# Performance work log

Hardware: AMD Instinct MI355X
Metric: run time of the kernel (lower is better)

The kernel has to match this reference:

```python
import jax, jax.numpy as jnp
import numpy as np

D_MODEL = 1024
NUM_HEADS = 16
HEAD_DIM = D_MODEL // NUM_HEADS


def setup_inputs() -> dict:
    key = jax.random.key(0)
    ks = jax.random.split(key, 5)
    x = jax.random.normal(ks[0], (2, 2048, D_MODEL), dtype=jnp.float32)
    # torch.nn.Linear default init ~ U(-1/sqrt(fan_in), 1/sqrt(fan_in)); scale roughly
    s = 1.0 / np.sqrt(D_MODEL)
    W_qkv = jax.random.uniform(ks[1], (D_MODEL, 3 * D_MODEL), jnp.float32, -s, s)
    b_qkv = jax.random.uniform(ks[2], (3 * D_MODEL,), jnp.float32, -s, s)
    W_out = jax.random.uniform(ks[3], (D_MODEL, D_MODEL), jnp.float32, -s, s)
    b_out = jax.random.uniform(ks[4], (D_MODEL,), jnp.float32, -s, s)
    return {"x": x, "W_qkv": W_qkv, "b_qkv": b_qkv, "W_out": W_out, "b_out": b_out}


def reference(x, W_qkv, b_qkv, W_out, b_out):
    B, S, D = x.shape
    H, Hd = NUM_HEADS, HEAD_DIM
    qkv = x @ W_qkv + b_qkv                      # [B,S,3D]
    q, k, v = jnp.split(qkv, 3, axis=-1)
    def split_heads(t):
        return t.reshape(B, S, H, Hd).transpose(0, 2, 1, 3)  # [B,H,S,Hd]
    q, k, v = split_heads(q), split_heads(k), split_heads(v)
    scores = jnp.einsum('bhqd,bhkd->bhqk', q, k) / jnp.sqrt(jnp.float32(Hd))
    weights = jax.nn.softmax(scores, axis=-1)
    attn = jnp.einsum('bhqk,bhkd->bhqd', weights, v)
    attn = attn.transpose(0, 2, 1, 3).reshape(B, S, D)
    return attn @ W_out + b_out
```

## Files before the change

### kernel.cpp

```cpp
#include <hip/hip_runtime.h>
#include <hip/hip_bf16.h>

#define DMODEL 1024
#define NH 16
#define HD 64
#define SEQ 2048
#define BATCH 2
#define BH (BATCH * NH)
#define MTOT (BATCH * SEQ)

typedef _Float16 f16x8 __attribute__((ext_vector_type(8)));
typedef _Float16 f16x4 __attribute__((ext_vector_type(4)));
typedef _Float16 f16x2 __attribute__((ext_vector_type(2)));
typedef float f32x4 __attribute__((ext_vector_type(4)));
typedef float f32x16 __attribute__((ext_vector_type(16)));

__device__ __forceinline__ void gload_lds16(const void* g, void* l) {
  __builtin_amdgcn_global_load_lds((const __attribute__((address_space(1))) unsigned*)g,
                                   (__attribute__((address_space(3))) unsigned*)l, 16, 0, 0);
}

__global__ __launch_bounds__(256) void cvt_f2h(const float* __restrict__ in,
                                               _Float16* __restrict__ out, int n8) {
  const int i = blockIdx.x * 256 + threadIdx.x;
  if (i < n8) {
    const float4 a = ((const float4*)in)[i * 2];
    const float4 b = ((const float4*)in)[i * 2 + 1];
    f16x8 o = {(_Float16)a.x, (_Float16)a.y, (_Float16)a.z, (_Float16)a.w,
               (_Float16)b.x, (_Float16)b.y, (_Float16)b.z, (_Float16)b.w};
    *(f16x8*)&out[(size_t)i * 8] = o;
  }
}

__global__ __launch_bounds__(256) void cvt_transpose(const float* __restrict__ W,
                                                     _Float16* __restrict__ Wt,
                                                     int N, int K) {
  __shared__ float Ls[64][65];
  const int k0 = blockIdx.y * 64, n0 = blockIdx.x * 64;
  const int t = threadIdx.x;
  const int r = t >> 2, c4 = (t & 3) * 16;
#pragma unroll
  for (int j = 0; j < 4; ++j) {
    const float4 v = *(const float4*)&W[(size_t)(k0 + r) * N + n0 + c4 + j * 4];
    Ls[r][c4 + j * 4 + 0] = v.x;
    Ls[r][c4 + j * 4 + 1] = v.y;
    Ls[r][c4 + j * 4 + 2] = v.z;
    Ls[r][c4 + j * 4 + 3] = v.w;
  }
  __syncthreads();
  f16x8 o0, o1;
#pragma unroll
  for (int j = 0; j < 8; ++j) {
    o0[j] = (_Float16)Ls[c4 + j][r];
    o1[j] = (_Float16)Ls[c4 + 8 + j][r];
  }
  *(f16x8*)&Wt[(size_t)(n0 + r) * K + k0 + c4] = o0;
  *(f16x8*)&Wt[(size_t)(n0 + r) * K + k0 + c4 + 8] = o1;
}

__global__ __launch_bounds__(256) void qkv_mm(const _Float16* __restrict__ A,
                                              const _Float16* __restrict__ Bt,
                                              const float* __restrict__ bias,
                                              _Float16* __restrict__ qh,
                                              _Float16* __restrict__ kh,
                                              _Float16* __restrict__ vh) {
  __shared__ __align__(16) _Float16 As[128 * 64];
  __shared__ __align__(16) _Float16 Bs[128 * 64];
  const int t = threadIdx.x;
  const int w = t >> 6, lane = t & 63;
  const int g = lane >> 4, lr = lane & 15;
  const int m0 = blockIdx.y * 128, n0 = blockIdx.x * 128;
  const int wr = w >> 1, wc = w & 1;
  const int srow = (lane >> 3);
  const int col8 = (lane & 7) * 8;
  f32x4 acc[4][4] = {};

  for (int k0 = 0; k0 < DMODEL; k0 += 64) {
    __syncthreads();
#pragma unroll
    for (int i = 0; i < 4; ++i) {
      const int row = w * 32 + i * 8 + srow;
      gload_lds16(A + (size_t)(m0 + row) * DMODEL + k0 + col8, &As[(w * 4 + i) * 512]);
      gload_lds16(Bt + (size_t)(n0 + row) * DMODEL + k0 + col8, &Bs[(w * 4 + i) * 512]);
    }
    __syncthreads();
#pragma unroll
    for (int ks = 0; ks < 2; ++ks) {
      f16x8 af[4], bf[4];
#pragma unroll
      for (int mi = 0; mi < 4; ++mi)
        af[mi] = *(const f16x8*)&As[(wr * 64 + mi * 16 + lr) * 64 + ks * 32 + g * 8];
#pragma unroll
      for (int ni = 0; ni < 4; ++ni)
        bf[ni] = *(const f16x8*)&Bs[(wc * 64 + ni * 16 + lr) * 64 + ks * 32 + g * 8];
#pragma unroll
      for (int mi = 0; mi < 4; ++mi)
#pragma unroll
        for (int ni = 0; ni < 4; ++ni)
          acc[mi][ni] = __builtin_amdgcn_mfma_f32_16x16x32_f16(af[mi], bf[ni], acc[mi][ni], 0, 0, 0);
    }
  }

#pragma unroll
  for (int ni = 0; ni < 4; ++ni) {
    const int n = n0 + wc * 64 + ni * 16 + lr;
    const float bn = bias[n];
    const int which = n >> 10, d = n & 1023, h = d >> 6, hd = d & 63;
    _Float16* dst = which == 0 ? qh : which == 1 ? kh : vh;
    const float scale = which == 0 ? 0.125f : 1.0f;
#pragma unroll
    for (int mi = 0; mi < 4; ++mi)
#pragma unroll
      for (int r = 0; r < 4; ++r) {
        const int m = m0 + wr * 64 + mi * 16 + g * 4 + r;
        const int bb = m >> 11, ss = m & 2047;
        dst[((size_t)(bb * NH + h) * SEQ + ss) * HD + hd] =
            (_Float16)((acc[mi][ni][r] + bn) * scale);
      }
  }
}

__global__ __launch_bounds__(256, 2) void attn_fused(const _Float16* __restrict__ qh,
                                                     const _Float16* __restrict__ kh,
                                                     const _Float16* __restrict__ vh,
                                                     _Float16* __restrict__ ao) {
  __shared__ __align__(16) _Float16 Vt[64][76];
  const int t = threadIdx.x;
  const int lane = t & 63, w = t >> 6;
  const int q = lane & 31, hi = lane >> 5;
  const int bh = blockIdx.y;
  const int q0 = blockIdx.x * 128 + w * 32;
  const _Float16* Qp = qh + (size_t)bh * SEQ * HD;
  const _Float16* Kp = kh + (size_t)bh * SEQ * HD;
  const _Float16* Vp = vh + (size_t)bh * SEQ * HD;

  f16x8 qf[4];
#pragma unroll
  for (int ks = 0; ks < 4; ++ks)
    qf[ks] = *(const f16x8*)(Qp + (size_t)(q0 + q) * HD + ks * 16 + hi * 8);

  f32x16 o0 = {}, o1 = {};
  float mrun = -3e30f, lrun = 0.f;

  const int skv = t & 63;
  const int sq4 = t >> 6;

  for (int kv0 = 0; kv0 < SEQ; kv0 += 64) {
    const f16x8 sv0 = *(const f16x8*)(Vp + (size_t)(kv0 + skv) * HD + sq4 * 16);
    const f16x8 sv1 = *(const f16x8*)(Vp + (size_t)(kv0 + skv) * HD + sq4 * 16 + 8);
    __syncthreads();
#pragma unroll
    for (int e = 0; e < 8; ++e) {
      Vt[sq4 * 16 + e][skv] = sv0[e];
      Vt[sq4 * 16 + 8 + e][skv] = sv1[e];
    }

    f32x16 s0 = {}, s1 = {};
#pragma unroll
    for (int ks = 0; ks < 4; ++ks) {
      const f16x8 k0 = *(const f16x8*)(Kp + (size_t)(kv0 + q) * HD + ks * 16 + hi * 8);
      const f16x8 k1 = *(const f16x8*)(Kp + (size_t)(kv0 + 32 + q) * HD + ks * 16 + hi * 8);
      s0 = __builtin_amdgcn_mfma_f32_32x32x16_f16(k0, qf[ks], s0, 0, 0, 0);
      s1 = __builtin_amdgcn_mfma_f32_32x32x16_f16(k1, qf[ks], s1, 0, 0, 0);
    }

    float tm[16];
#pragma unroll
    for (int r = 0; r < 16; ++r) tm[r] = fmaxf(s0[r], s1[r]);
#pragma unroll
    for (int d = 8; d > 0; d >>= 1)
#pragma unroll
      for (int r = 0; r < d; ++r) tm[r] = fmaxf(tm[r], tm[r + d]);
    float mx = fmaxf(tm[0], __shfl_xor(tm[0], 32));
    const float mnew = fmaxf(mrun, mx);
    const float corr = __expf(mrun - mnew);
    mrun = mnew;
#pragma unroll
    for (int r = 0; r < 16; ++r) {
      s0[r] = __expf(s0[r] - mnew);
      s1[r] = __expf(s1[r] - mnew);
    }
    float ts[16];
#pragma unroll
    for (int r = 0; r < 16; ++r) ts[r] = s0[r] + s1[r];
#pragma unroll
    for (int d = 8; d > 0; d >>= 1)
#pragma unroll
      for (int r = 0; r < d; ++r) ts[r] += ts[r + d];
    float rs = ts[0] + __shfl_xor(ts[0], 32);
    lrun = lrun * corr + rs;
#pragma unroll
    for (int r = 0; r < 16; ++r) {
      o0[r] *= corr;
      o1[r] *= corr;
    }

    __syncthreads();

#pragma unroll
    for (int ks = 0; ks < 4; ++ks) {
      const int base = 8 * (ks & 1);
      unsigned u0, u1, u2, u3;
#pragma unroll
      for (int w01 = 0; w01 < 2; ++w01) {
        float a0, a1, b0, b1;
        if (ks < 2) {
          a0 = s0[base + 2 * w01];     a1 = s0[base + 2 * w01 + 1];
          b0 = s0[base + 4 + 2 * w01]; b1 = s0[base + 4 + 2 * w01 + 1];
        } else {
          a0 = s1[base + 2 * w01];     a1 = s1[base + 2 * w01 + 1];
          b0 = s1[base + 4 + 2 * w01]; b1 = s1[base + 4 + 2 * w01 + 1];
        }
        f16x2 hm0; hm0[0] = (_Float16)a0; hm0[1] = (_Float16)a1;
        f16x2 hm1; hm1[0] = (_Float16)b0; hm1[1] = (_Float16)b1;
        unsigned Pm0, Pm1;
        __builtin_memcpy(&Pm0, &hm0, 4);
        __builtin_memcpy(&Pm1, &hm1, 4);
        const unsigned local = hi ? Pm1 : Pm0;
        const unsigned sent = hi ? Pm0 : Pm1;
        const unsigned cross = __shfl_xor(sent, 32);
        const unsigned wa = hi ? cross : local;
        const unsigned wb = hi ? local : cross;
        if (w01 == 0) { u0 = wa; u2 = wb; } else { u1 = wa; u3 = wb; }
      }
      unsigned ww[4] = {u0, u1, u2, u3};
      f16x8 pb;
      __builtin_memcpy(&pb, ww, 16);
      const f16x8 va0 = *(const f16x8*)&Vt[0 + q][ks * 16 + hi * 8];
      const f16x8 va1 = *(const f16x8*)&Vt[32 + q][ks * 16 + hi * 8];
      o0 = __builtin_amdgcn_mfma_f32_32x32x16_f16(va0, pb, o0, 0, 0, 0);
      o1 = __builtin_amdgcn_mfma_f32_32x32x16_f16(va1, pb, o1, 0, 0, 0);
    }
  }

  const float invl = 1.0f / lrun;
  _Float16* aob = ao + (size_t)bh * SEQ * HD + (size_t)(q0 + q) * HD;
#pragma unroll
  for (int m = 0; m < 4; ++m) {
    f16x4 v0, v1;
#pragma unroll
    for (int s2 = 0; s2 < 4; ++s2) {
      v0[s2] = (_Float16)(o0[4 * m + s2] * invl);
      v1[s2] = (_Float16)(o1[4 * m + s2] * invl);
    }
    *(f16x4*)(aob + 8 * m + 4 * hi) = v0;
    *(f16x4*)(aob + 32 + 8 * m + 4 * hi) = v1;
  }
}

__global__ __launch_bounds__(256) void out_mm(const _Float16* __restrict__ Ah,
                                              const _Float16* __restrict__ Bt,
                                              const float* __restrict__ bias,
                                              float* __restrict__ out) {
  __shared__ __align__(16) _Float16 As[128 * 64];
  __shared__ __align__(16) _Float16 Bs[128 * 64];
  const int t = threadIdx.x;
  const int w = t >> 6, lane = t & 63;
  const int g = lane >> 4, lr = lane & 15;
  const int m0 = blockIdx.y * 128, n0 = blockIdx.x * 128;
  const int wr = w >> 1, wc = w & 1;
  const int srow = (lane >> 3);
  const int col8 = (lane & 7) * 8;
  f32x4 acc[4][4] = {};

  for (int k0 = 0; k0 < DMODEL; k0 += 64) {
    const int h = k0 >> 6;
    __syncthreads();
#pragma unroll
    for (int i = 0; i < 4; ++i) {
      const int row = w * 32 + i * 8 + srow;
      const int m = m0 + row;
      const int bb = m >> 11, ss = m & 2047;
      gload_lds16(Ah + ((size_t)(bb * NH + h) * SEQ + ss) * HD + col8, &As[(w * 4 + i) * 512]);
      gload_lds16(Bt + (size_t)(n0 + row) * DMODEL + k0 + col8, &Bs[(w * 4 + i) * 512]);
    }
    __syncthreads();
#pragma unroll
    for (int ks = 0; ks < 2; ++ks) {
      f16x8 af[4], bf[4];
#pragma unroll
      for (int mi = 0; mi < 4; ++mi)
        af[mi] = *(const f16x8*)&As[(wr * 64 + mi * 16 + lr) * 64 + ks * 32 + g * 8];
#pragma unroll
      for (int ni = 0; ni < 4; ++ni)
        bf[ni] = *(const f16x8*)&Bs[(wc * 64 + ni * 16 + lr) * 64 + ks * 32 + g * 8];
#pragma unroll
      for (int mi = 0; mi < 4; ++mi)
#pragma unroll
        for (int ni = 0; ni < 4; ++ni)
          acc[mi][ni] = __builtin_amdgcn_mfma_f32_16x16x32_f16(af[mi], bf[ni], acc[mi][ni], 0, 0, 0);
    }
  }

#pragma unroll
  for (int ni = 0; ni < 4; ++ni) {
    const int n = n0 + wc * 64 + ni * 16 + lr;
    const float bn = bias[n];
#pragma unroll
    for (int mi = 0; mi < 4; ++mi)
#pragma unroll
      for (int r = 0; r < 4; ++r) {
        const int m = m0 + wr * 64 + mi * 16 + g * 4 + r;
        out[(size_t)m * DMODEL + n] = acc[mi][ni][r] + bn;
      }
  }
}

extern "C" void kernel_launch(void* const* d_in, const int* in_sizes, int n_in,
                              void* d_out, int out_size, void* d_ws, size_t ws_size,
                              hipStream_t stream) {
  const float* x = (const float*)d_in[0];
  const float* Wqkv = (const float*)d_in[1];
  const float* bqkv = (const float*)d_in[2];
  const float* Wout = (const float*)d_in[3];
  const float* bout = (const float*)d_in[4];
  float* out = (float*)d_out;

  char* ws = (char*)d_ws;
  const size_t MB = 1u << 20;
  _Float16* Xh = (_Float16*)(ws);
  _Float16* qh = (_Float16*)(ws + 8 * MB);
  _Float16* kh = (_Float16*)(ws + 16 * MB);
  _Float16* vh = (_Float16*)(ws + 24 * MB);
  _Float16* Wtq = (_Float16*)(ws + 32 * MB);
  _Float16* Wto = (_Float16*)(ws + 38 * MB + 512 * 1024);
  _Float16* attnh = Xh;

  cvt_f2h<<<dim3(MTOT * DMODEL / 8 / 256), 256, 0, stream>>>(x, Xh, MTOT * DMODEL / 8);
  cvt_transpose<<<dim3(3072 / 64, DMODEL / 64), 256, 0, stream>>>(Wqkv, Wtq, 3072, DMODEL);
  cvt_transpose<<<dim3(DMODEL / 64, DMODEL / 64), 256, 0, stream>>>(Wout, Wto, DMODEL, DMODEL);
  qkv_mm<<<dim3(3072 / 128, MTOT / 128), 256, 0, stream>>>(Xh, Wtq, bqkv, qh, kh, vh);
  attn_fused<<<dim3(SEQ / 128, BH), 256, 0, stream>>>(qh, kh, vh, attnh);
  out_mm<<<dim3(DMODEL / 128, MTOT / 128), 256, 0, stream>>>(attnh, Wto, bout, out);
}
```

Before: 253.9 us.

## Software-pipeline attention loop with double-buffered V and K prefetch in registers

Restructures the attention kernel's KV loop into a two-stage ping-pong. The next tile's K and V are prefetched into registers while the current tile's QK^T and softmax run, and V is double-buffered in LDS, leaving one barrier per tile instead of two. The Q scale now folds in log2(e) so exp2f replaces __expf, and the running max is only rescaled when a block's max exceeds it by more than a threshold (lazy rescaling). s_setprio is also raised around the MFMA groups. In exchange the kernel holds many more prefetch registers, which may reduce occupancy, and the lazy rescale lets unnormalized exponentials grow up to 2^8.

```diff
diff --git a/kernel.cpp b/kernel.cpp
--- a/kernel.cpp
+++ b/kernel.cpp
@@ -107,7 +107,7 @@
     const float bn = bias[n];
     const int which = n >> 10, d = n & 1023, h = d >> 6, hd = d & 63;
     _Float16* dst = which == 0 ? qh : which == 1 ? kh : vh;
-    const float scale = which == 0 ? 0.125f : 1.0f;
+    const float scale = which == 0 ? 0.18033688011f : 1.0f;
 #pragma unroll
     for (int mi = 0; mi < 4; ++mi)
 #pragma unroll
@@ -120,11 +120,125 @@
   }
 }
 
+__device__ __forceinline__ void load_k(const _Float16* Kp, int kv0, int q, int hi,
+                                       f16x8 (&kr)[8]) {
+#pragma unroll
+  for (int ks = 0; ks < 4; ++ks) {
+    kr[2 * ks] = *(const f16x8*)(Kp + (size_t)(kv0 + q) * HD + ks * 16 + hi * 8);
+    kr[2 * ks + 1] = *(const f16x8*)(Kp + (size_t)(kv0 + 32 + q) * HD + ks * 16 + hi * 8);
+  }
+}
+
+__device__ __forceinline__ void load_v(const _Float16* Vp, int kv0, int skv, int sq4,
+                                       f16x8 (&vr)[2]) {
+  vr[0] = *(const f16x8*)(Vp + (size_t)(kv0 + skv) * HD + sq4 * 16);
+  vr[1] = *(const f16x8*)(Vp + (size_t)(kv0 + skv) * HD + sq4 * 16 + 8);
+}
+
+__device__ __forceinline__ void store_v(_Float16 (*Vt)[76], int skv, int sq4,
+                                        const f16x8 (&vr)[2]) {
+#pragma unroll
+  for (int e = 0; e < 8; ++e) {
+    Vt[sq4 * 16 + e][skv] = vr[0][e];
+    Vt[sq4 * 16 + 8 + e][skv] = vr[1][e];
+  }
+}
+
+__device__ __forceinline__ void qkt(const f16x8 (&kr)[8], const f16x8 (&qf)[4],
+                                    f32x16& s0, f32x16& s1) {
+  s0 = {};
+  s1 = {};
+  __builtin_amdgcn_s_setprio(1);
+#pragma unroll
+  for (int ks = 0; ks < 4; ++ks) {
+    s0 = __builtin_amdgcn_mfma_f32_32x32x16_f16(kr[2 * ks], qf[ks], s0, 0, 0, 0);
+    s1 = __builtin_amdgcn_mfma_f32_32x32x16_f16(kr[2 * ks + 1], qf[ks], s1, 0, 0, 0);
+  }
+  __builtin_amdgcn_s_setprio(0);
+}
+
+__device__ __forceinline__ void softmax_update(f32x16& s0, f32x16& s1, float& mrun,
+                                               float& lrun, f32x16& o0, f32x16& o1) {
+  float tm[16];
+#pragma unroll
+  for (int r = 0; r < 16; ++r) tm[r] = fmaxf(s0[r], s1[r]);
+#pragma unroll
+  for (int d = 8; d > 0; d >>= 1)
+#pragma unroll
+    for (int r = 0; r < d; ++r) tm[r] = fmaxf(tm[r], tm[r + d]);
+  const float mx = fmaxf(tm[0], __shfl_xor(tm[0], 32));
+  if (!__all(mx <= mrun + 8.0f)) {
+    const float mnew = fmaxf(mrun, mx);
+    const float corr = exp2f(mrun - mnew);
+    mrun = mnew;
+    lrun *= corr;
+#pragma unroll
+    for (int r = 0; r < 16; ++r) {
+      o0[r] *= corr;
+      o1[r] *= corr;
+    }
+  }
+#pragma unroll
+  for (int r = 0; r < 16; ++r) {
+    s0[r] = exp2f(s0[r] - mrun);
+    s1[r] = exp2f(s1[r] - mrun);
+  }
+  float ts[16];
+#pragma unroll
+  for (int r = 0; r < 16; ++r) ts[r] = s0[r] + s1[r];
+#pragma unroll
+  for (int d = 8; d > 0; d >>= 1)
+#pragma unroll
+    for (int r = 0; r < d; ++r) ts[r] += ts[r + d];
+  lrun += ts[0] + __shfl_xor(ts[0], 32);
+}
+
+__device__ __forceinline__ void pv(const f32x16& s0, const f32x16& s1,
+                                   const _Float16 (*Vt)[76], int q, int hi,
+                                   f32x16& o0, f32x16& o1) {
+#pragma unroll
+  for (int ks = 0; ks < 4; ++ks) {
+    const int base = 8 * (ks & 1);
+    unsigned u0, u1, u2, u3;
+#pragma unroll
+    for (int w01 = 0; w01 < 2; ++w01) {
+      float a0, a1, b0, b1;
+      if (ks < 2) {
+        a0 = s0[base + 2 * w01];     a1 = s0[base + 2 * w01 + 1];
+        b0 = s0[base + 4 + 2 * w01]; b1 = s0[base + 4 + 2 * w01 + 1];
+      } else {
+        a0 = s1[base + 2 * w01];     a1 = s1[base + 2 * w01 + 1];
+        b0 = s1[base + 4 + 2 * w01]; b1 = s1[base + 4 + 2 * w01 + 1];
+      }
+      f16x2 hm0; hm0[0] = (_Float16)a0; hm0[1] = (_Float16)a1;
+      f16x2 hm1; hm1[0] = (_Float16)b0; hm1[1] = (_Float16)b1;
+      unsigned Pm0, Pm1;
+      __builtin_memcpy(&Pm0, &hm0, 4);
+      __builtin_memcpy(&Pm1, &hm1, 4);
+      const unsigned local = hi ? Pm1 : Pm0;
+      const unsigned sent = hi ? Pm0 : Pm1;
+      const unsigned cross = __shfl_xor(sent, 32);
+      const unsigned wa = hi ? cross : local;
+      const unsigned wb = hi ? local : cross;
+      if (w01 == 0) { u0 = wa; u2 = wb; } else { u1 = wa; u3 = wb; }
+    }
+    unsigned ww[4] = {u0, u1, u2, u3};
+    f16x8 pb;
+    __builtin_memcpy(&pb, ww, 16);
+    const f16x8 va0 = *(const f16x8*)&Vt[0 + q][ks * 16 + hi * 8];
+    const f16x8 va1 = *(const f16x8*)&Vt[32 + q][ks * 16 + hi * 8];
+    __builtin_amdgcn_s_setprio(1);
+    o0 = __builtin_amdgcn_mfma_f32_32x32x16_f16(va0, pb, o0, 0, 0, 0);
+    o1 = __builtin_amdgcn_mfma_f32_32x32x16_f16(va1, pb, o1, 0, 0, 0);
+    __builtin_amdgcn_s_setprio(0);
+  }
+}
+
 __global__ __launch_bounds__(256, 2) void attn_fused(const _Float16* __restrict__ qh,
                                                      const _Float16* __restrict__ kh,
                                                      const _Float16* __restrict__ vh,
                                                      _Float16* __restrict__ ao) {
-  __shared__ __align__(16) _Float16 Vt[64][76];
+  __shared__ __align__(16) _Float16 Vt[2][64][76];
   const int t = threadIdx.x;
   const int lane = t & 63, w = t >> 6;
   const int q = lane & 31, hi = lane >> 5;
@@ -139,98 +253,37 @@
   for (int ks = 0; ks < 4; ++ks)
     qf[ks] = *(const f16x8*)(Qp + (size_t)(q0 + q) * HD + ks * 16 + hi * 8);
 
+  const int skv = t & 63;
+  const int sq4 = t >> 6;
+
+  f16x8 kA[8], kB[8], vA[2], vB[2];
+  load_v(Vp, 0, skv, sq4, vA);
+  load_k(Kp, 0, q, hi, kA);
+  store_v(Vt[0], skv, sq4, vA);
+
   f32x16 o0 = {}, o1 = {};
   float mrun = -3e30f, lrun = 0.f;
-
-  const int skv = t & 63;
-  const int sq4 = t >> 6;
-
-  for (int kv0 = 0; kv0 < SEQ; kv0 += 64) {
-    const f16x8 sv0 = *(const f16x8*)(Vp + (size_t)(kv0 + skv) * HD + sq4 * 16);
-    const f16x8 sv1 = *(const f16x8*)(Vp + (size_t)(kv0 + skv) * HD + sq4 * 16 + 8);
-    __syncthreads();
-#pragma unroll
-    for (int e = 0; e < 8; ++e) {
-      Vt[sq4 * 16 + e][skv] = sv0[e];
-      Vt[sq4 * 16 + 8 + e][skv] = sv1[e];
-    }
-
-    f32x16 s0 = {}, s1 = {};
-#pragma unroll
-    for (int ks = 0; ks < 4; ++ks) {
-      const f16x8 k0 = *(const f16x8*)(Kp + (size_t)(kv0 + q) * HD + ks * 16 + hi * 8);
-      const f16x8 k1 = *(const f16x8*)(Kp + (size_t)(kv0 + 32 + q) * HD + ks * 16 + hi * 8);
-      s0 = __builtin_amdgcn_mfma_f32_32x32x16_f16(k0, qf[ks], s0, 0, 0, 0);
-      s1 = __builtin_amdgcn_mfma_f32_32x32x16_f16(k1, qf[ks], s1, 0, 0, 0);
-    }
-
-    float tm[16];
-#pragma unroll
-    for (int r = 0; r < 16; ++r) tm[r] = fmaxf(s0[r], s1[r]);
-#pragma unroll
-    for (int d = 8; d > 0; d >>= 1)
-#pragma unroll
-      for (int r = 0; r < d; ++r) tm[r] = fmaxf(tm[r], tm[r + d]);
-    float mx = fmaxf(tm[0], __shfl_xor(tm[0], 32));
-    const float mnew = fmaxf(mrun, mx);
-    const float corr = __expf(mrun - mnew);
-    mrun = mnew;
-#pragma unroll
-    for (int r = 0; r < 16; ++r) {
-      s0[r] = __expf(s0[r] - mnew);
-      s1[r] = __expf(s1[r] - mnew);
-    }
-    float ts[16];
-#pragma unroll
-    for (int r = 0; r < 16; ++r) ts[r] = s0[r] + s1[r];
-#pragma unroll
-    for (int d = 8; d > 0; d >>= 1)
-#pragma unroll
-      for (int r = 0; r < d; ++r) ts[r] += ts[r + d];
-    float rs = ts[0] + __shfl_xor(ts[0], 32);
-    lrun = lrun * corr + rs;
-#pragma unroll
-    for (int r = 0; r < 16; ++r) {
-      o0[r] *= corr;
-      o1[r] *= corr;
-    }
-
-    __syncthreads();
-
-#pragma unroll
-    for (int ks = 0; ks < 4; ++ks) {
-      const int base = 8 * (ks & 1);
-      unsigned u0, u1, u2, u3;
-#pragma unroll
-      for (int w01 = 0; w01 < 2; ++w01) {
-        float a0, a1, b0, b1;
-        if (ks < 2) {
-          a0 = s0[base + 2 * w01];     a1 = s0[base + 2 * w01 + 1];
-          b0 = s0[base + 4 + 2 * w01]; b1 = s0[base + 4 + 2 * w01 + 1];
-        } else {
-          a0 = s1[base + 2 * w01];     a1 = s1[base + 2 * w01 + 1];
-          b0 = s1[base + 4 + 2 * w01]; b1 = s1[base + 4 + 2 * w01 + 1];
-        }
-        f16x2 hm0; hm0[0] = (_Float16)a0; hm0[1] = (_Float16)a1;
-        f16x2 hm1; hm1[0] = (_Float16)b0; hm1[1] = (_Float16)b1;
-        unsigned Pm0, Pm1;
-        __builtin_memcpy(&Pm0, &hm0, 4);
-        __builtin_memcpy(&Pm1, &hm1, 4);
-        const unsigned local = hi ? Pm1 : Pm0;
-        const unsigned sent = hi ? Pm0 : Pm1;
-        const unsigned cross = __shfl_xor(sent, 32);
-        const unsigned wa = hi ? cross : local;
-        const unsigned wb = hi ? local : cross;
-        if (w01 == 0) { u0 = wa; u2 = wb; } else { u1 = wa; u3 = wb; }
-      }
-      unsigned ww[4] = {u0, u1, u2, u3};
-      f16x8 pb;
-      __builtin_memcpy(&pb, ww, 16);
-      const f16x8 va0 = *(const f16x8*)&Vt[0 + q][ks * 16 + hi * 8];
-      const f16x8 va1 = *(const f16x8*)&Vt[32 + q][ks * 16 + hi * 8];
-      o0 = __builtin_amdgcn_mfma_f32_32x32x16_f16(va0, pb, o0, 0, 0, 0);
-      o1 = __builtin_amdgcn_mfma_f32_32x32x16_f16(va1, pb, o1, 0, 0, 0);
-    }
+  f32x16 s0, s1;
+
+#pragma unroll 1
+  for (int t2 = 0; t2 < 16; ++t2) {
+    const int kvE = t2 * 128;
+    qkt(kA, qf, s0, s1);
+    load_v(Vp, kvE + 64, skv, sq4, vB);
+    load_k(Kp, kvE + 64, q, hi, kB);
+    softmax_update(s0, s1, mrun, lrun, o0, o1);
+    __syncthreads();
+    store_v(Vt[1], skv, sq4, vB);
+    pv(s0, s1, Vt[0], q, hi, o0, o1);
+    qkt(kB, qf, s0, s1);
+    if (t2 < 15) {
+      load_v(Vp, kvE + 128, skv, sq4, vA);
+      load_k(Kp, kvE + 128, q, hi, kA);
+    }
+    softmax_update(s0, s1, mrun, lrun, o0, o1);
+    __syncthreads();
+    if (t2 < 15) store_v(Vt[0], skv, sq4, vA);
+    pv(s0, s1, Vt[1], q, hi, o0, o1);
   }
 
   const float invl = 1.0f / lrun;
```

Result: slower. 268.5 us (+5.7%).
